# Performance work log

Measured on AMD Instinct MI355X. Metric: run time of the kernel, lower is better.

The kernel has to match this reference:

```python
import jax, jax.numpy as jnp
import numpy as np


def setup_inputs() -> dict:
    key = jax.random.key(0)
    ks = jax.random.split(key, 8)
    B, D_MODEL, H, W, S = 32, 512, 64, 64, 64
    L = H * W
    D_INNER = D_MODEL  # ssd_expand = 1
    x = jax.random.normal(ks[0], (B, D_MODEL, L), jnp.float32)
    # BCdt_proj: Conv1d(d_model -> 3*state_dim, k=1) with bias
    w_bcdt = jax.random.normal(ks[1], (3 * S, D_MODEL), jnp.float32) / np.float32(np.sqrt(D_MODEL))
    b_bcdt = jnp.zeros((3 * S,), jnp.float32)
    # dw_conv: depthwise Conv2d(3*S -> 3*S, k=3, pad=1, groups=3*S) with bias
    w_dw = jax.random.normal(ks[2], (3 * S, 1, 3, 3), jnp.float32) / np.float32(3.0)
    b_dw = jnp.zeros((3 * S,), jnp.float32)
    # hz_proj: Conv1d(d_model -> 2*d_inner, k=1) with bias
    w_hz = jax.random.normal(ks[3], (2 * D_INNER, D_MODEL), jnp.float32) / np.float32(np.sqrt(D_MODEL))
    b_hz = jnp.zeros((2 * D_INNER,), jnp.float32)
    # out_proj: Conv1d(d_inner -> d_model, k=1) with bias
    w_out = jax.random.normal(ks[4], (D_MODEL, D_INNER), jnp.float32) / np.float32(np.sqrt(D_INNER))
    b_out = jnp.zeros((D_MODEL,), jnp.float32)
    A = jax.random.uniform(ks[5], (S,), jnp.float32, minval=1.0, maxval=16.0)
    Dskip = jnp.ones((1,), jnp.float32)
    return {"x": x, "w_bcdt": w_bcdt, "b_bcdt": b_bcdt, "w_dw": w_dw, "b_dw": b_dw,
            "w_hz": w_hz, "b_hz": b_hz, "w_out": w_out, "b_out": b_out,
            "A": A, "Dskip": Dskip, "H": H, "W": W}


def reference(x, w_bcdt, b_bcdt, w_dw, b_dw, w_hz, b_hz, w_out, b_out, A, Dskip, H, W):
    Bn, Cin, L = x.shape
    S = A.shape[0]
    d_inner = w_out.shape[1]
    # pointwise BCdt projection: [B, 3S, L]
    bcdt = jnp.einsum('bcl,oc->bol', x, w_bcdt) + b_bcdt[None, :, None]
    # depthwise 3x3 conv over spatial view
    bcdt = bcdt.reshape(Bn, 3 * S, H, W)
    bcdt = jax.lax.conv_general_dilated(
        bcdt, w_dw, window_strides=(1, 1), padding=((1, 1), (1, 1)),
        dimension_numbers=('NCHW', 'OIHW', 'NCHW'), feature_group_count=3 * S)
    bcdt = bcdt + b_dw[None, :, None, None]
    bcdt = bcdt.reshape(Bn, 3 * S, L)
    Bm, Cm, dt = jnp.split(bcdt, 3, axis=1)  # each [B, S, L]
    Asm = jax.nn.softmax(dt + A[None, :, None], axis=-1)  # softmax over length
    AB = Asm * Bm  # [B, S, L]
    # h = x @ AB^T : [B, d_model, S]
    h = jnp.einsum('bcl,bsl->bcs', x, AB)
    hz = jnp.einsum('bcs,oc->bos', h, w_hz) + b_hz[None, :, None]  # [B, 2*d_inner, S]
    h1, z = jnp.split(hz, 2, axis=1)
    hg = h1 * jax.nn.silu(z) + h1 * Dskip  # gated + D-skip
    ho = jnp.einsum('bcs,oc->bos', hg, w_out) + b_out[None, :, None]  # [B, d_model, S]
    # y = h @ C : [B, d_model, L] -> [B, d_model, H, W]
    y = jnp.einsum('bcs,bsl->bcl', ho, Cm).reshape(Bn, -1, H, W)
    return y, ho
```

## Files before the change

### kernel.cpp

```cpp
#include <hip/hip_runtime.h>

constexpr int BN = 32;
constexpr int DM = 512;
constexpr int SD = 64;
constexpr int LL = 4096;
constexpr int C3 = 192;

#define OUTER16(acc, a4, b4)                                               \
    acc[0][0] += a4.x * b4.x; acc[0][1] += a4.x * b4.y;                    \
    acc[0][2] += a4.x * b4.z; acc[0][3] += a4.x * b4.w;                    \
    acc[1][0] += a4.y * b4.x; acc[1][1] += a4.y * b4.y;                    \
    acc[1][2] += a4.y * b4.z; acc[1][3] += a4.y * b4.w;                    \
    acc[2][0] += a4.z * b4.x; acc[2][1] += a4.z * b4.y;                    \
    acc[2][2] += a4.z * b4.z; acc[2][3] += a4.z * b4.w;                    \
    acc[3][0] += a4.w * b4.x; acc[3][1] += a4.w * b4.y;                    \
    acc[3][2] += a4.w * b4.z; acc[3][3] += a4.w * b4.w;

__global__ __launch_bounds__(256) void k1_bcdt(const float* __restrict__ x,
                                               const float* __restrict__ w,
                                               const float* __restrict__ bias,
                                               float* __restrict__ out) {
    int b = blockIdx.z, o0 = blockIdx.y * 64, l0 = blockIdx.x * 64;
    __shared__ float wl[16][64];
    __shared__ float xl[16][64];
    int t = threadIdx.x;
    int tx = t & 15, ty = t >> 4;
    float acc[4][4] = {};
    const float* xb = x + (size_t)b * DM * LL;
    int oi = t >> 2, kkw = (t & 3) * 4;
    int ci = t >> 4, li = (t & 15) * 4;
    for (int k0 = 0; k0 < DM; k0 += 16) {
        float4 wv = *(const float4*)&w[(size_t)(o0 + oi) * DM + k0 + kkw];
        float4 xv = *(const float4*)&xb[(size_t)(k0 + ci) * LL + l0 + li];
        wl[kkw + 0][oi] = wv.x; wl[kkw + 1][oi] = wv.y;
        wl[kkw + 2][oi] = wv.z; wl[kkw + 3][oi] = wv.w;
        *(float4*)&xl[ci][li] = xv;
        __syncthreads();
#pragma unroll
        for (int kk = 0; kk < 16; ++kk) {
            float4 a4 = *(const float4*)&wl[kk][ty * 4];
            float4 b4 = *(const float4*)&xl[kk][tx * 4];
            OUTER16(acc, a4, b4)
        }
        __syncthreads();
    }
#pragma unroll
    for (int r = 0; r < 4; ++r) {
        float bo = bias[o0 + ty * 4 + r];
        float4 v = make_float4(acc[r][0] + bo, acc[r][1] + bo, acc[r][2] + bo, acc[r][3] + bo);
        *(float4*)&out[((size_t)b * C3 + o0 + ty * 4 + r) * LL + l0 + tx * 4] = v;
    }
}

__global__ __launch_bounds__(256) void k2_conv(float* __restrict__ buf,
                                               const float* __restrict__ wdw,
                                               const float* __restrict__ bdw,
                                               float* __restrict__ cmws) {
    int bc = blockIdx.x;
    int b = bc / C3, ch = bc % C3;
    __shared__ float p[66 * 66];
    int t = threadIdx.x;
    for (int i = t; i < 66 * 66; i += 256) p[i] = 0.f;
    __syncthreads();
    float* plane = buf + (size_t)bc * LL;
    for (int i = t; i < 4096; i += 256) {
        int yy = i >> 6, xx = i & 63;
        p[(yy + 1) * 66 + (xx + 1)] = plane[i];
    }
    __syncthreads();
    float wv[9];
#pragma unroll
    for (int k = 0; k < 9; ++k) wv[k] = wdw[ch * 9 + k];
    float bias = bdw[ch];
    bool is_cm = (ch >= 64 && ch < 128);
    float* cmp = is_cm ? (cmws + ((size_t)b * SD + (ch - 64)) * LL) : nullptr;
    for (int i = t; i < 4096; i += 256) {
        int yy = i >> 6, xx = i & 63;
        float a = bias;
#pragma unroll
        for (int ky = 0; ky < 3; ++ky)
#pragma unroll
            for (int kx = 0; kx < 3; ++kx)
                a += wv[ky * 3 + kx] * p[(yy + ky) * 66 + (xx + kx)];
        plane[i] = a;
        if (is_cm) cmp[i] = a;
    }
}

__global__ __launch_bounds__(256) void k3_softmax(float* __restrict__ conv,
                                                  const float* __restrict__ Ap) {
    int bs = blockIdx.x;
    int b = bs >> 6, s = bs & 63;
    const float* dt = conv + ((size_t)b * C3 + 128 + s) * LL;
    float* bm = conv + ((size_t)b * C3 + s) * LL;
    float Av = Ap[s];
    int t = threadIdx.x;
    float v[16];
    float mx = -1e30f;
#pragma unroll
    for (int j = 0; j < 16; ++j) { v[j] = dt[j * 256 + t] + Av; mx = fmaxf(mx, v[j]); }
#pragma unroll
    for (int off = 32; off >= 1; off >>= 1) mx = fmaxf(mx, __shfl_xor(mx, off, 64));
    __shared__ float redm[4], reds[4];
    int wid = t >> 6, lane = t & 63;
    if (lane == 0) redm[wid] = mx;
    __syncthreads();
    mx = fmaxf(fmaxf(redm[0], redm[1]), fmaxf(redm[2], redm[3]));
    float sum = 0.f;
#pragma unroll
    for (int j = 0; j < 16; ++j) { v[j] = expf(v[j] - mx); sum += v[j]; }
#pragma unroll
    for (int off = 32; off >= 1; off >>= 1) sum += __shfl_xor(sum, off, 64);
    if (lane == 0) reds[wid] = sum;
    __syncthreads();
    sum = reds[0] + reds[1] + reds[2] + reds[3];
    float inv = 1.f / sum;
#pragma unroll
    for (int j = 0; j < 16; ++j) {
        float bmv = bm[j * 256 + t];
        bm[j * 256 + t] = v[j] * inv * bmv;
    }
}

__global__ __launch_bounds__(256) void k4_h(const float* __restrict__ x,
                                            const float* __restrict__ conv,
                                            float* __restrict__ h) {
    int b = blockIdx.y, c0 = blockIdx.x * 64;
    __shared__ float xl[16][64];
    __shared__ float al[16][64];
    int t = threadIdx.x, tx = t & 15, ty = t >> 4;
    float acc[4][4] = {};
    const float* xb = x + (size_t)b * DM * LL;
    const float* abb = conv + (size_t)b * C3 * LL;
    int ri = t >> 2, kk4 = (t & 3) * 4;
    for (int k0 = 0; k0 < LL; k0 += 16) {
        float4 xv = *(const float4*)&xb[(size_t)(c0 + ri) * LL + k0 + kk4];
        float4 av = *(const float4*)&abb[(size_t)ri * LL + k0 + kk4];
        xl[kk4 + 0][ri] = xv.x; xl[kk4 + 1][ri] = xv.y;
        xl[kk4 + 2][ri] = xv.z; xl[kk4 + 3][ri] = xv.w;
        al[kk4 + 0][ri] = av.x; al[kk4 + 1][ri] = av.y;
        al[kk4 + 2][ri] = av.z; al[kk4 + 3][ri] = av.w;
        __syncthreads();
#pragma unroll
        for (int kk = 0; kk < 16; ++kk) {
            float4 a4 = *(const float4*)&xl[kk][ty * 4];
            float4 b4 = *(const float4*)&al[kk][tx * 4];
            OUTER16(acc, a4, b4)
        }
        __syncthreads();
    }
#pragma unroll
    for (int r = 0; r < 4; ++r)
        *(float4*)&h[((size_t)b * DM + c0 + ty * 4 + r) * SD + tx * 4] =
            make_float4(acc[r][0], acc[r][1], acc[r][2], acc[r][3]);
}

__global__ __launch_bounds__(256) void k5_hz_gate(const float* __restrict__ w,
                                                  const float* __restrict__ bias,
                                                  const float* __restrict__ h,
                                                  const float* __restrict__ dskip,
                                                  float* __restrict__ hg) {
    int b = blockIdx.y, o0 = blockIdx.x * 64;
    __shared__ float wl1[16][64];
    __shared__ float wl2[16][64];
    __shared__ float hl[16][64];
    int t = threadIdx.x, tx = t & 15, ty = t >> 4;
    float acc1[4][4] = {}, acc2[4][4] = {};
    const float* hb = h + (size_t)b * DM * SD;
    int oi = t >> 2, kkw = (t & 3) * 4;
    int kh = t >> 4, sh = (t & 15) * 4;
    for (int k0 = 0; k0 < DM; k0 += 16) {
        float4 w1 = *(const float4*)&w[(size_t)(o0 + oi) * DM + k0 + kkw];
        float4 w2 = *(const float4*)&w[(size_t)(o0 + 512 + oi) * DM + k0 + kkw];
        wl1[kkw + 0][oi] = w1.x; wl1[kkw + 1][oi] = w1.y;
        wl1[kkw + 2][oi] = w1.z; wl1[kkw + 3][oi] = w1.w;
        wl2[kkw + 0][oi] = w2.x; wl2[kkw + 1][oi] = w2.y;
        wl2[kkw + 2][oi] = w2.z; wl2[kkw + 3][oi] = w2.w;
        *(float4*)&hl[kh][sh] = *(const float4*)&hb[(size_t)(k0 + kh) * SD + sh];
        __syncthreads();
#pragma unroll
        for (int kk = 0; kk < 16; ++kk) {
            float4 b4 = *(const float4*)&hl[kk][tx * 4];
            float4 a4 = *(const float4*)&wl1[kk][ty * 4];
            OUTER16(acc1, a4, b4)
            float4 c4 = *(const float4*)&wl2[kk][ty * 4];
            OUTER16(acc2, c4, b4)
        }
        __syncthreads();
    }
    float d = dskip[0];
#pragma unroll
    for (int r = 0; r < 4; ++r) {
        int o = o0 + ty * 4 + r;
        float b1 = bias[o], b2 = bias[o + 512];
        float4 v;
        float* vp = &v.x;
#pragma unroll
        for (int j = 0; j < 4; ++j) {
            float h1 = acc1[r][j] + b1;
            float z  = acc2[r][j] + b2;
            float sig = 1.f / (1.f + expf(-z));
            vp[j] = h1 * (z * sig + d);
        }
        *(float4*)&hg[((size_t)b * DM + o) * SD + tx * 4] = v;
    }
}

__global__ __launch_bounds__(256) void k5c_out(const float* __restrict__ w,
                                               const float* __restrict__ bias,
                                               const float* __restrict__ hg,
                                               float* __restrict__ ho_out) {
    int b = blockIdx.y, o0 = blockIdx.x * 64;
    __shared__ float wl[16][64];
    __shared__ float hl[16][64];
    int t = threadIdx.x, tx = t & 15, ty = t >> 4;
    float acc[4][4] = {};
    const float* hb = hg + (size_t)b * DM * SD;
    int oi = t >> 2, kkw = (t & 3) * 4;
    int kh = t >> 4, sh = (t & 15) * 4;
    for (int k0 = 0; k0 < DM; k0 += 16) {
        float4 wv = *(const float4*)&w[(size_t)(o0 + oi) * DM + k0 + kkw];
        wl[kkw + 0][oi] = wv.x; wl[kkw + 1][oi] = wv.y;
        wl[kkw + 2][oi] = wv.z; wl[kkw + 3][oi] = wv.w;
        *(float4*)&hl[kh][sh] = *(const float4*)&hb[(size_t)(k0 + kh) * SD + sh];
        __syncthreads();
#pragma unroll
        for (int kk = 0; kk < 16; ++kk) {
            float4 a4 = *(const float4*)&wl[kk][ty * 4];
            float4 b4 = *(const float4*)&hl[kk][tx * 4];
            OUTER16(acc, a4, b4)
        }
        __syncthreads();
    }
#pragma unroll
    for (int r = 0; r < 4; ++r) {
        int o = o0 + ty * 4 + r;
        float bo = bias[o];
        float4 v = make_float4(acc[r][0] + bo, acc[r][1] + bo, acc[r][2] + bo, acc[r][3] + bo);
        *(float4*)&ho_out[((size_t)b * DM + o) * SD + tx * 4] = v;
    }
}

__global__ __launch_bounds__(256) void k6_y(const float* __restrict__ ho,
                                            const float* __restrict__ cmws,
                                            float* __restrict__ y) {
    int b = blockIdx.z, c0 = blockIdx.y * 64, l0 = blockIdx.x * 64;
    __shared__ float hl[16][64];
    __shared__ float cl[16][64];
    int t = threadIdx.x, tx = t & 15, ty = t >> 4;
    float acc[4][4] = {};
    const float* hb = ho + (size_t)b * DM * SD;
    const float* cm = cmws + (size_t)b * SD * LL;
    int ci = t >> 2, kkh = (t & 3) * 4;
    int kc = t >> 4, li = (t & 15) * 4;
    for (int k0 = 0; k0 < SD; k0 += 16) {
        float4 hv = *(const float4*)&hb[(size_t)(c0 + ci) * SD + k0 + kkh];
        hl[kkh + 0][ci] = hv.x; hl[kkh + 1][ci] = hv.y;
        hl[kkh + 2][ci] = hv.z; hl[kkh + 3][ci] = hv.w;
        *(float4*)&cl[kc][li] = *(const float4*)&cm[(size_t)(k0 + kc) * LL + l0 + li];
        __syncthreads();
#pragma unroll
        for (int kk = 0; kk < 16; ++kk) {
            float4 a4 = *(const float4*)&hl[kk][ty * 4];
            float4 b4 = *(const float4*)&cl[kk][tx * 4];
            OUTER16(acc, a4, b4)
        }
        __syncthreads();
    }
#pragma unroll
    for (int r = 0; r < 4; ++r)
        *(float4*)&y[((size_t)b * DM + c0 + ty * 4 + r) * LL + l0 + tx * 4] =
            make_float4(acc[r][0], acc[r][1], acc[r][2], acc[r][3]);
}

extern "C" void kernel_launch(void* const* d_in, const int* in_sizes, int n_in,
                              void* d_out, int out_size, void* d_ws, size_t ws_size,
                              hipStream_t stream) {
    const float* x      = (const float*)d_in[0];
    const float* w_bcdt = (const float*)d_in[1];
    const float* b_bcdt = (const float*)d_in[2];
    const float* w_dw   = (const float*)d_in[3];
    const float* b_dw   = (const float*)d_in[4];
    const float* w_hz   = (const float*)d_in[5];
    const float* b_hz   = (const float*)d_in[6];
    const float* w_out  = (const float*)d_in[7];
    const float* b_out  = (const float*)d_in[8];
    const float* A      = (const float*)d_in[9];
    const float* Dskip  = (const float*)d_in[10];

    float* y_out  = (float*)d_out;
    float* ho_out = y_out + (size_t)BN * DM * LL;

    float* conv = y_out;

    char* ws = (char*)d_ws;
    float* cmws = (float*)(ws + 0);
    float* h    = (float*)(ws + 33554432);
    float* hg   = (float*)(ws + 37748736);

    k1_bcdt<<<dim3(64, 3, 32), 256, 0, stream>>>(x, w_bcdt, b_bcdt, conv);
    k2_conv<<<dim3(BN * C3), 256, 0, stream>>>(conv, w_dw, b_dw, cmws);
    k3_softmax<<<dim3(BN * SD), 256, 0, stream>>>(conv, A);
    k4_h<<<dim3(8, BN), 256, 0, stream>>>(x, conv, h);
    k5_hz_gate<<<dim3(8, BN), 256, 0, stream>>>(w_hz, b_hz, h, Dskip, hg);
    k5c_out<<<dim3(8, BN), 256, 0, stream>>>(w_out, b_out, hg, ho_out);
    k6_y<<<dim3(64, 8, BN), 256, 0, stream>>>(ho_out, cmws, y_out);
}
```

Measured before the change: 1.149 ms.

## Split-K the h GEMM, enlarge k1 tiles with prefetch, vectorize depthwise conv

The x·AB^T reduction over L is split into 8 partial blocks per (batch, channel tile), with a separate kernel summing the partials. The aim is to fix the original 256-block launch, which underfills the GPU. k1 and k4 now compute 64x128 tiles with register prefetch of the next K slice to hide global latency. The depthwise conv loads and stores float4 and reuses a 3x6 register window per 4 outputs, and it zeroes only the halo. The partial buffer is placed in y_out scratch space that k6 later overwrites, and the split-K adds an extra reduction pass over 8 partial copies.

Result: faster. 1.058 ms (-8.0%).

```diff
diff --git a/kernel.cpp b/kernel.cpp
--- a/kernel.cpp
+++ b/kernel.cpp
@@ -20,35 +20,59 @@
                                                const float* __restrict__ w,
                                                const float* __restrict__ bias,
                                                float* __restrict__ out) {
-    int b = blockIdx.z, o0 = blockIdx.y * 64, l0 = blockIdx.x * 64;
-    __shared__ float wl[16][64];
-    __shared__ float xl[16][64];
+    int b = blockIdx.z, o0 = blockIdx.y * 64, l0 = blockIdx.x * 128;
+    __shared__ float wl[32][68];
+    __shared__ float xl[32][128];
     int t = threadIdx.x;
     int tx = t & 15, ty = t >> 4;
-    float acc[4][4] = {};
+    float acc0[4][4] = {}, acc1[4][4] = {};
     const float* xb = x + (size_t)b * DM * LL;
     int oi = t >> 2, kkw = (t & 3) * 4;
-    int ci = t >> 4, li = (t & 15) * 4;
-    for (int k0 = 0; k0 < DM; k0 += 16) {
-        float4 wv = *(const float4*)&w[(size_t)(o0 + oi) * DM + k0 + kkw];
-        float4 xv = *(const float4*)&xb[(size_t)(k0 + ci) * LL + l0 + li];
-        wl[kkw + 0][oi] = wv.x; wl[kkw + 1][oi] = wv.y;
-        wl[kkw + 2][oi] = wv.z; wl[kkw + 3][oi] = wv.w;
-        *(float4*)&xl[ci][li] = xv;
-        __syncthreads();
-#pragma unroll
-        for (int kk = 0; kk < 16; ++kk) {
+    int ci = t >> 5, li = (t & 31) * 4;
+    float4 wv0 = *(const float4*)&w[(size_t)(o0 + oi) * DM + kkw];
+    float4 wv1 = *(const float4*)&w[(size_t)(o0 + oi) * DM + kkw + 16];
+    float4 xv0 = *(const float4*)&xb[(size_t)(ci +  0) * LL + l0 + li];
+    float4 xv1 = *(const float4*)&xb[(size_t)(ci +  8) * LL + l0 + li];
+    float4 xv2 = *(const float4*)&xb[(size_t)(ci + 16) * LL + l0 + li];
+    float4 xv3 = *(const float4*)&xb[(size_t)(ci + 24) * LL + l0 + li];
+    for (int k0 = 0; k0 < DM; k0 += 32) {
+        wl[kkw +  0][oi] = wv0.x; wl[kkw +  1][oi] = wv0.y;
+        wl[kkw +  2][oi] = wv0.z; wl[kkw +  3][oi] = wv0.w;
+        wl[kkw + 16][oi] = wv1.x; wl[kkw + 17][oi] = wv1.y;
+        wl[kkw + 18][oi] = wv1.z; wl[kkw + 19][oi] = wv1.w;
+        *(float4*)&xl[ci +  0][li] = xv0;
+        *(float4*)&xl[ci +  8][li] = xv1;
+        *(float4*)&xl[ci + 16][li] = xv2;
+        *(float4*)&xl[ci + 24][li] = xv3;
+        __syncthreads();
+        if (k0 + 32 < DM) {
+            const float* wp = &w[(size_t)(o0 + oi) * DM + k0 + 32 + kkw];
+            wv0 = *(const float4*)wp;
+            wv1 = *(const float4*)(wp + 16);
+            const float* xp = &xb[(size_t)(k0 + 32 + ci) * LL + l0 + li];
+            xv0 = *(const float4*)xp;
+            xv1 = *(const float4*)(xp + (size_t)8 * LL);
+            xv2 = *(const float4*)(xp + (size_t)16 * LL);
+            xv3 = *(const float4*)(xp + (size_t)24 * LL);
+        }
+#pragma unroll
+        for (int kk = 0; kk < 32; ++kk) {
             float4 a4 = *(const float4*)&wl[kk][ty * 4];
             float4 b4 = *(const float4*)&xl[kk][tx * 4];
-            OUTER16(acc, a4, b4)
+            float4 c4 = *(const float4*)&xl[kk][64 + tx * 4];
+            OUTER16(acc0, a4, b4)
+            OUTER16(acc1, a4, c4)
         }
         __syncthreads();
     }
 #pragma unroll
     for (int r = 0; r < 4; ++r) {
         float bo = bias[o0 + ty * 4 + r];
-        float4 v = make_float4(acc[r][0] + bo, acc[r][1] + bo, acc[r][2] + bo, acc[r][3] + bo);
-        *(float4*)&out[((size_t)b * C3 + o0 + ty * 4 + r) * LL + l0 + tx * 4] = v;
+        float* op = &out[((size_t)b * C3 + o0 + ty * 4 + r) * LL + l0];
+        *(float4*)&op[tx * 4] =
+            make_float4(acc0[r][0] + bo, acc0[r][1] + bo, acc0[r][2] + bo, acc0[r][3] + bo);
+        *(float4*)&op[64 + tx * 4] =
+            make_float4(acc1[r][0] + bo, acc1[r][1] + bo, acc1[r][2] + bo, acc1[r][3] + bo);
     }
 }
 
@@ -60,12 +84,15 @@
     int b = bc / C3, ch = bc % C3;
     __shared__ float p[66 * 66];
     int t = threadIdx.x;
-    for (int i = t; i < 66 * 66; i += 256) p[i] = 0.f;
-    __syncthreads();
+    for (int i = t; i < 66; i += 256) { p[i] = 0.f; p[65 * 66 + i] = 0.f; }
+    for (int i = t; i < 64; i += 256) { p[(i + 1) * 66] = 0.f; p[(i + 1) * 66 + 65] = 0.f; }
     float* plane = buf + (size_t)bc * LL;
-    for (int i = t; i < 4096; i += 256) {
-        int yy = i >> 6, xx = i & 63;
-        p[(yy + 1) * 66 + (xx + 1)] = plane[i];
+    const float4* plane4 = (const float4*)plane;
+    for (int i = t; i < 1024; i += 256) {
+        float4 v = plane4[i];
+        int yy = i >> 4, xx = (i & 15) << 2;
+        float* dst = &p[(yy + 1) * 66 + xx + 1];
+        dst[0] = v.x; dst[1] = v.y; dst[2] = v.z; dst[3] = v.w;
     }
     __syncthreads();
     float wv[9];
@@ -74,16 +101,26 @@
     float bias = bdw[ch];
     bool is_cm = (ch >= 64 && ch < 128);
     float* cmp = is_cm ? (cmws + ((size_t)b * SD + (ch - 64)) * LL) : nullptr;
-    for (int i = t; i < 4096; i += 256) {
-        int yy = i >> 6, xx = i & 63;
-        float a = bias;
-#pragma unroll
-        for (int ky = 0; ky < 3; ++ky)
-#pragma unroll
-            for (int kx = 0; kx < 3; ++kx)
-                a += wv[ky * 3 + kx] * p[(yy + ky) * 66 + (xx + kx)];
-        plane[i] = a;
-        if (is_cm) cmp[i] = a;
+    for (int i = t; i < 1024; i += 256) {
+        int yy = i >> 4, xx = (i & 15) << 2;
+        float r0[6], r1[6], r2[6];
+#pragma unroll
+        for (int j = 0; j < 6; ++j) {
+            r0[j] = p[(yy + 0) * 66 + xx + j];
+            r1[j] = p[(yy + 1) * 66 + xx + j];
+            r2[j] = p[(yy + 2) * 66 + xx + j];
+        }
+        float4 o;
+        float* op = &o.x;
+#pragma unroll
+        for (int j = 0; j < 4; ++j) {
+            op[j] = bias
+                  + wv[0] * r0[j] + wv[1] * r0[j + 1] + wv[2] * r0[j + 2]
+                  + wv[3] * r1[j] + wv[4] * r1[j + 1] + wv[5] * r1[j + 2]
+                  + wv[6] * r2[j] + wv[7] * r2[j + 1] + wv[8] * r2[j + 2];
+        }
+        ((float4*)plane)[i] = o;
+        if (is_cm) ((float4*)cmp)[i] = o;
     }
 }
 
@@ -122,37 +159,68 @@
     }
 }
 
+constexpr int KP = 512;
+constexpr size_t HP_STRIDE = (size_t)BN * DM * SD;
 __global__ __launch_bounds__(256) void k4_h(const float* __restrict__ x,
                                             const float* __restrict__ conv,
-                                            float* __restrict__ h) {
-    int b = blockIdx.y, c0 = blockIdx.x * 64;
-    __shared__ float xl[16][64];
-    __shared__ float al[16][64];
+                                            float* __restrict__ hpart) {
+    int b = blockIdx.z, c0 = blockIdx.x * 128, part = blockIdx.y;
+    int kbeg = part * KP;
+    __shared__ float xl[16][132];
+    __shared__ float al[16][68];
     int t = threadIdx.x, tx = t & 15, ty = t >> 4;
-    float acc[4][4] = {};
+    float acc0[4][4] = {}, acc1[4][4] = {};
     const float* xb = x + (size_t)b * DM * LL;
     const float* abb = conv + (size_t)b * C3 * LL;
     int ri = t >> 2, kk4 = (t & 3) * 4;
-    for (int k0 = 0; k0 < LL; k0 += 16) {
-        float4 xv = *(const float4*)&xb[(size_t)(c0 + ri) * LL + k0 + kk4];
-        float4 av = *(const float4*)&abb[(size_t)ri * LL + k0 + kk4];
-        xl[kk4 + 0][ri] = xv.x; xl[kk4 + 1][ri] = xv.y;
-        xl[kk4 + 2][ri] = xv.z; xl[kk4 + 3][ri] = xv.w;
+    float4 xv0 = *(const float4*)&xb[(size_t)(c0 + ri) * LL + kbeg + kk4];
+    float4 xv1 = *(const float4*)&xb[(size_t)(c0 + 64 + ri) * LL + kbeg + kk4];
+    float4 av  = *(const float4*)&abb[(size_t)ri * LL + kbeg + kk4];
+    for (int k0 = kbeg; k0 < kbeg + KP; k0 += 16) {
+        xl[kk4 + 0][ri] = xv0.x; xl[kk4 + 1][ri] = xv0.y;
+        xl[kk4 + 2][ri] = xv0.z; xl[kk4 + 3][ri] = xv0.w;
+        xl[kk4 + 0][64 + ri] = xv1.x; xl[kk4 + 1][64 + ri] = xv1.y;
+        xl[kk4 + 2][64 + ri] = xv1.z; xl[kk4 + 3][64 + ri] = xv1.w;
         al[kk4 + 0][ri] = av.x; al[kk4 + 1][ri] = av.y;
         al[kk4 + 2][ri] = av.z; al[kk4 + 3][ri] = av.w;
         __syncthreads();
+        if (k0 + 16 < kbeg + KP) {
+            xv0 = *(const float4*)&xb[(size_t)(c0 + ri) * LL + k0 + 16 + kk4];
+            xv1 = *(const float4*)&xb[(size_t)(c0 + 64 + ri) * LL + k0 + 16 + kk4];
+            av  = *(const float4*)&abb[(size_t)ri * LL + k0 + 16 + kk4];
+        }
 #pragma unroll
         for (int kk = 0; kk < 16; ++kk) {
             float4 a4 = *(const float4*)&xl[kk][ty * 4];
+            float4 c4 = *(const float4*)&xl[kk][64 + ty * 4];
             float4 b4 = *(const float4*)&al[kk][tx * 4];
-            OUTER16(acc, a4, b4)
-        }
-        __syncthreads();
-    }
-#pragma unroll
-    for (int r = 0; r < 4; ++r)
-        *(float4*)&h[((size_t)b * DM + c0 + ty * 4 + r) * SD + tx * 4] =
-            make_float4(acc[r][0], acc[r][1], acc[r][2], acc[r][3]);
+            OUTER16(acc0, a4, b4)
+            OUTER16(acc1, c4, b4)
+        }
+        __syncthreads();
+    }
+    float* hp = hpart + (size_t)part * HP_STRIDE;
+#pragma unroll
+    for (int r = 0; r < 4; ++r) {
+        *(float4*)&hp[((size_t)b * DM + c0 + ty * 4 + r) * SD + tx * 4] =
+            make_float4(acc0[r][0], acc0[r][1], acc0[r][2], acc0[r][3]);
+        *(float4*)&hp[((size_t)b * DM + c0 + 64 + ty * 4 + r) * SD + tx * 4] =
+            make_float4(acc1[r][0], acc1[r][1], acc1[r][2], acc1[r][3]);
+    }
+}
+
+__global__ __launch_bounds__(256) void k4r(const float* __restrict__ hpart,
+                                           float* __restrict__ h) {
+    size_t i = (size_t)blockIdx.x * 256 + threadIdx.x;
+    const float4* hp = (const float4*)hpart;
+    constexpr size_t PS = HP_STRIDE / 4;
+    float4 a = hp[i];
+#pragma unroll
+    for (int p = 1; p < 8; ++p) {
+        float4 v = hp[i + (size_t)p * PS];
+        a.x += v.x; a.y += v.y; a.z += v.z; a.w += v.w;
+    }
+    ((float4*)h)[i] = a;
 }
 
 __global__ __launch_bounds__(256) void k5_hz_gate(const float* __restrict__ w,
@@ -293,15 +361,18 @@
 
     float* conv = y_out;
 
+    float* hpart = y_out + (size_t)33554432;
+
     char* ws = (char*)d_ws;
     float* cmws = (float*)(ws + 0);
     float* h    = (float*)(ws + 33554432);
     float* hg   = (float*)(ws + 37748736);
 
-    k1_bcdt<<<dim3(64, 3, 32), 256, 0, stream>>>(x, w_bcdt, b_bcdt, conv);
+    k1_bcdt<<<dim3(32, 3, 32), 256, 0, stream>>>(x, w_bcdt, b_bcdt, conv);
     k2_conv<<<dim3(BN * C3), 256, 0, stream>>>(conv, w_dw, b_dw, cmws);
     k3_softmax<<<dim3(BN * SD), 256, 0, stream>>>(conv, A);
-    k4_h<<<dim3(8, BN), 256, 0, stream>>>(x, conv, h);
+    k4_h<<<dim3(4, 8, BN), 256, 0, stream>>>(x, conv, hpart);
+    k4r<<<dim3(1024), 256, 0, stream>>>(hpart, h);
     k5_hz_gate<<<dim3(8, BN), 256, 0, stream>>>(w_hz, b_hz, h, Dskip, hg);
     k5c_out<<<dim3(8, BN), 256, 0, stream>>>(w_out, b_out, hg, ho_out);
     k6_y<<<dim3(64, 8, BN), 256, 0, stream>>>(ho_out, cmws, y_out);
```

## Rewrite pipeline with 8x8 register tiles, split-K h GEMM, fused conv+softmax

Applied to the files above, without the earlier changes.

Nearly every kernel is rewritten. The GEMMs (bcdt projection, h, y) now use 8x8 per-thread register tiles with swizzled, padded shared memory and register prefetch of the next K slice. The h reduction is split along L into 16 partial sums plus a separate reduce kernel, so many more blocks run at once. The depthwise conv and softmax are fused into one kernel per (b,s), removing a round trip of the plane through global memory. The gate is moved into the out-projection's load. Partial sums and hz scratch live inside the y output buffer, which is only overwritten later, and the extra reduce pass adds memory traffic.

Result: slower. 1.220 ms (+6.2%).

```diff
diff --git a/kernel.cpp b/kernel.cpp
--- a/kernel.cpp
+++ b/kernel.cpp
@@ -16,206 +16,281 @@
     acc[3][0] += a4.w * b4.x; acc[3][1] += a4.w * b4.y;                    \
     acc[3][2] += a4.w * b4.z; acc[3][3] += a4.w * b4.w;
 
+#define OUTER64(acc, a0, a1, b0, b1)                                       \
+    {                                                                      \
+        float af[8] = {a0.x, a0.y, a0.z, a0.w, a1.x, a1.y, a1.z, a1.w};    \
+        float bf[8] = {b0.x, b0.y, b0.z, b0.w, b1.x, b1.y, b1.z, b1.w};    \
+        _Pragma("unroll")                                                  \
+        for (int i_ = 0; i_ < 8; ++i_)                                     \
+            _Pragma("unroll")                                              \
+            for (int j_ = 0; j_ < 8; ++j_) acc[i_][j_] += af[i_] * bf[j_]; \
+    }
+
 __global__ __launch_bounds__(256) void k1_bcdt(const float* __restrict__ x,
                                                const float* __restrict__ w,
                                                const float* __restrict__ bias,
                                                float* __restrict__ out) {
-    int b = blockIdx.z, o0 = blockIdx.y * 64, l0 = blockIdx.x * 64;
-    __shared__ float wl[16][64];
-    __shared__ float xl[16][64];
+    int o0 = blockIdx.x * 64;
+    int l0 = blockIdx.y * 256;
+    int b  = blockIdx.z;
+    __shared__ float  wl[16][68];
+    __shared__ float4 xl4[16][66];
     int t = threadIdx.x;
-    int tx = t & 15, ty = t >> 4;
-    float acc[4][4] = {};
+    int tx = t & 31, ty = t >> 5;
+    float acc[8][8] = {};
     const float* xb = x + (size_t)b * DM * LL;
-    int oi = t >> 2, kkw = (t & 3) * 4;
-    int ci = t >> 4, li = (t & 15) * 4;
+
+    int wo = t & 63, wk = t >> 6;
+    int kr = t >> 4, cbase = t & 15;
+    int wpos[4];
+#pragma unroll
+    for (int j = 0; j < 4; ++j) {
+        int cb = cbase + 16 * j, pb = cb >> 1;
+        wpos[j] = ((pb ^ ((pb >> 2) & 3)) << 1) | (cb & 1);
+    }
+    int rp = (tx ^ ((tx >> 2) & 3)) * 2;
+
+    float4 wv = *(const float4*)&w[(size_t)(o0 + wo) * DM + wk * 4];
+    float4 xv[4];
+#pragma unroll
+    for (int j = 0; j < 4; ++j)
+        xv[j] = *(const float4*)&xb[(size_t)kr * LL + l0 + (cbase + 16 * j) * 4];
+
     for (int k0 = 0; k0 < DM; k0 += 16) {
-        float4 wv = *(const float4*)&w[(size_t)(o0 + oi) * DM + k0 + kkw];
-        float4 xv = *(const float4*)&xb[(size_t)(k0 + ci) * LL + l0 + li];
-        wl[kkw + 0][oi] = wv.x; wl[kkw + 1][oi] = wv.y;
-        wl[kkw + 2][oi] = wv.z; wl[kkw + 3][oi] = wv.w;
-        *(float4*)&xl[ci][li] = xv;
-        __syncthreads();
+        wl[wk * 4 + 0][wo] = wv.x; wl[wk * 4 + 1][wo] = wv.y;
+        wl[wk * 4 + 2][wo] = wv.z; wl[wk * 4 + 3][wo] = wv.w;
+#pragma unroll
+        for (int j = 0; j < 4; ++j) xl4[kr][wpos[j]] = xv[j];
+        __syncthreads();
+        if (k0 + 16 < DM) {
+            wv = *(const float4*)&w[(size_t)(o0 + wo) * DM + k0 + 16 + wk * 4];
+#pragma unroll
+            for (int j = 0; j < 4; ++j)
+                xv[j] = *(const float4*)&xb[(size_t)(k0 + 16 + kr) * LL + l0 + (cbase + 16 * j) * 4];
+        }
 #pragma unroll
         for (int kk = 0; kk < 16; ++kk) {
-            float4 a4 = *(const float4*)&wl[kk][ty * 4];
-            float4 b4 = *(const float4*)&xl[kk][tx * 4];
-            OUTER16(acc, a4, b4)
-        }
-        __syncthreads();
-    }
-#pragma unroll
-    for (int r = 0; r < 4; ++r) {
-        float bo = bias[o0 + ty * 4 + r];
-        float4 v = make_float4(acc[r][0] + bo, acc[r][1] + bo, acc[r][2] + bo, acc[r][3] + bo);
-        *(float4*)&out[((size_t)b * C3 + o0 + ty * 4 + r) * LL + l0 + tx * 4] = v;
-    }
-}
-
-__global__ __launch_bounds__(256) void k2_conv(float* __restrict__ buf,
-                                               const float* __restrict__ wdw,
-                                               const float* __restrict__ bdw,
-                                               float* __restrict__ cmws) {
-    int bc = blockIdx.x;
-    int b = bc / C3, ch = bc % C3;
+            float4 a0 = *(const float4*)&wl[kk][ty * 8];
+            float4 a1 = *(const float4*)&wl[kk][ty * 8 + 4];
+            float4 b0 = xl4[kk][rp];
+            float4 b1 = xl4[kk][rp + 1];
+            OUTER64(acc, a0, a1, b0, b1)
+        }
+        __syncthreads();
+    }
+#pragma unroll
+    for (int i = 0; i < 8; ++i) {
+        int o = o0 + ty * 8 + i;
+        float bo = bias[o];
+        float* op = &out[((size_t)b * C3 + o) * LL + l0 + tx * 8];
+        *(float4*)&op[0] = make_float4(acc[i][0] + bo, acc[i][1] + bo, acc[i][2] + bo, acc[i][3] + bo);
+        *(float4*)&op[4] = make_float4(acc[i][4] + bo, acc[i][5] + bo, acc[i][6] + bo, acc[i][7] + bo);
+    }
+}
+
+__device__ __forceinline__ void load_plane(const float* __restrict__ plane, float* p, int t) {
+    const float4* p4 = (const float4*)plane;
+    for (int i = t; i < 1024; i += 256) {
+        float4 v = p4[i];
+        int yy = i >> 4, xx = (i & 15) << 2;
+        float* dst = &p[(yy + 1) * 66 + xx + 1];
+        dst[0] = v.x; dst[1] = v.y; dst[2] = v.z; dst[3] = v.w;
+    }
+}
+
+__device__ __forceinline__ void conv_plane(const float* p, const float* wv, float bias,
+                                           int t, float4* out4) {
+#pragma unroll
+    for (int g = 0; g < 4; ++g) {
+        int fi = g * 256 + t;
+        int yy = fi >> 4, xx = (fi & 15) << 2;
+        float r0[6], r1[6], r2[6];
+#pragma unroll
+        for (int j = 0; j < 6; ++j) {
+            r0[j] = p[(yy + 0) * 66 + xx + j];
+            r1[j] = p[(yy + 1) * 66 + xx + j];
+            r2[j] = p[(yy + 2) * 66 + xx + j];
+        }
+        float* op = (float*)&out4[g];
+#pragma unroll
+        for (int j = 0; j < 4; ++j)
+            op[j] = bias + wv[0] * r0[j] + wv[1] * r0[j + 1] + wv[2] * r0[j + 2]
+                         + wv[3] * r1[j] + wv[4] * r1[j + 1] + wv[5] * r1[j + 2]
+                         + wv[6] * r2[j] + wv[7] * r2[j + 1] + wv[8] * r2[j + 2];
+    }
+}
+
+__global__ __launch_bounds__(256) void k2_fused(float* __restrict__ buf,
+                                                const float* __restrict__ wdw,
+                                                const float* __restrict__ bdw,
+                                                const float* __restrict__ Ap,
+                                                float* __restrict__ cmws) {
+    int s = blockIdx.x, b = blockIdx.y;
     __shared__ float p[66 * 66];
+    __shared__ float redm[4], reds[4];
     int t = threadIdx.x;
-    for (int i = t; i < 66 * 66; i += 256) p[i] = 0.f;
-    __syncthreads();
-    float* plane = buf + (size_t)bc * LL;
-    for (int i = t; i < 4096; i += 256) {
-        int yy = i >> 6, xx = i & 63;
-        p[(yy + 1) * 66 + (xx + 1)] = plane[i];
-    }
-    __syncthreads();
-    float wv[9];
-#pragma unroll
-    for (int k = 0; k < 9; ++k) wv[k] = wdw[ch * 9 + k];
-    float bias = bdw[ch];
-    bool is_cm = (ch >= 64 && ch < 128);
-    float* cmp = is_cm ? (cmws + ((size_t)b * SD + (ch - 64)) * LL) : nullptr;
-    for (int i = t; i < 4096; i += 256) {
-        int yy = i >> 6, xx = i & 63;
-        float a = bias;
-#pragma unroll
-        for (int ky = 0; ky < 3; ++ky)
-#pragma unroll
-            for (int kx = 0; kx < 3; ++kx)
-                a += wv[ky * 3 + kx] * p[(yy + ky) * 66 + (xx + kx)];
-        plane[i] = a;
-        if (is_cm) cmp[i] = a;
-    }
-}
-
-__global__ __launch_bounds__(256) void k3_softmax(float* __restrict__ conv,
-                                                  const float* __restrict__ Ap) {
-    int bs = blockIdx.x;
-    int b = bs >> 6, s = bs & 63;
-    const float* dt = conv + ((size_t)b * C3 + 128 + s) * LL;
-    float* bm = conv + ((size_t)b * C3 + s) * LL;
+    for (int i = t; i < 66; i += 256) { p[i] = 0.f; p[65 * 66 + i] = 0.f; }
+    for (int i = t; i < 64; i += 256) { p[(i + 1) * 66] = 0.f; p[(i + 1) * 66 + 65] = 0.f; }
+
+    const float* base = buf + (size_t)b * C3 * LL;
+    float wvB[9], wvC[9], wvD[9];
+#pragma unroll
+    for (int k = 0; k < 9; ++k) {
+        wvB[k] = wdw[(size_t)s * 9 + k];
+        wvC[k] = wdw[(size_t)(64 + s) * 9 + k];
+        wvD[k] = wdw[(size_t)(128 + s) * 9 + k];
+    }
+    float4 bm4[4], cm4[4], dt4[4];
+
+    load_plane(base + (size_t)s * LL, p, t);
+    __syncthreads();
+    conv_plane(p, wvB, bdw[s], t, bm4);
+    __syncthreads();
+    load_plane(base + (size_t)(64 + s) * LL, p, t);
+    __syncthreads();
+    conv_plane(p, wvC, bdw[64 + s], t, cm4);
+    __syncthreads();
+    {
+        float4* cmp4 = (float4*)(cmws + ((size_t)b * SD + s) * LL);
+#pragma unroll
+        for (int g = 0; g < 4; ++g) cmp4[g * 256 + t] = cm4[g];
+    }
+    load_plane(base + (size_t)(128 + s) * LL, p, t);
+    __syncthreads();
+    conv_plane(p, wvD, bdw[128 + s], t, dt4);
+
     float Av = Ap[s];
-    int t = threadIdx.x;
-    float v[16];
     float mx = -1e30f;
 #pragma unroll
-    for (int j = 0; j < 16; ++j) { v[j] = dt[j * 256 + t] + Av; mx = fmaxf(mx, v[j]); }
+    for (int g = 0; g < 4; ++g) {
+        float* v = (float*)&dt4[g];
+#pragma unroll
+        for (int j = 0; j < 4; ++j) { v[j] += Av; mx = fmaxf(mx, v[j]); }
+    }
 #pragma unroll
     for (int off = 32; off >= 1; off >>= 1) mx = fmaxf(mx, __shfl_xor(mx, off, 64));
-    __shared__ float redm[4], reds[4];
     int wid = t >> 6, lane = t & 63;
     if (lane == 0) redm[wid] = mx;
     __syncthreads();
     mx = fmaxf(fmaxf(redm[0], redm[1]), fmaxf(redm[2], redm[3]));
     float sum = 0.f;
 #pragma unroll
-    for (int j = 0; j < 16; ++j) { v[j] = expf(v[j] - mx); sum += v[j]; }
+    for (int g = 0; g < 4; ++g) {
+        float* v = (float*)&dt4[g];
+#pragma unroll
+        for (int j = 0; j < 4; ++j) { v[j] = expf(v[j] - mx); sum += v[j]; }
+    }
 #pragma unroll
     for (int off = 32; off >= 1; off >>= 1) sum += __shfl_xor(sum, off, 64);
     if (lane == 0) reds[wid] = sum;
     __syncthreads();
     sum = reds[0] + reds[1] + reds[2] + reds[3];
     float inv = 1.f / sum;
-#pragma unroll
-    for (int j = 0; j < 16; ++j) {
-        float bmv = bm[j * 256 + t];
-        bm[j * 256 + t] = v[j] * inv * bmv;
-    }
-}
-
+    float4* abp4 = (float4*)(buf + ((size_t)b * C3 + s) * LL);
+#pragma unroll
+    for (int g = 0; g < 4; ++g) {
+        float4 bm = bm4[g], dt = dt4[g], o;
+        o.x = dt.x * inv * bm.x; o.y = dt.y * inv * bm.y;
+        o.z = dt.z * inv * bm.z; o.w = dt.w * inv * bm.w;
+        abp4[g * 256 + t] = o;
+    }
+}
+
+constexpr int KP4 = 256;
+constexpr size_t HP_STRIDE = (size_t)BN * DM * SD;
 __global__ __launch_bounds__(256) void k4_h(const float* __restrict__ x,
                                             const float* __restrict__ conv,
-                                            float* __restrict__ h) {
-    int b = blockIdx.y, c0 = blockIdx.x * 64;
-    __shared__ float xl[16][64];
-    __shared__ float al[16][64];
-    int t = threadIdx.x, tx = t & 15, ty = t >> 4;
-    float acc[4][4] = {};
+                                            float* __restrict__ hpart) {
+    int c0 = blockIdx.x * 256;
+    int part = blockIdx.y;
+    int b = blockIdx.z;
+    int kbeg = part * KP4;
+    __shared__ float xlf[16][264];
+    __shared__ float al[16][68];
+    int t = threadIdx.x;
+    int tc = t & 31, ts = t >> 5;
+    float acc[8][8] = {};
     const float* xb = x + (size_t)b * DM * LL;
     const float* abb = conv + (size_t)b * C3 * LL;
-    int ri = t >> 2, kk4 = (t & 3) * 4;
-    for (int k0 = 0; k0 < LL; k0 += 16) {
-        float4 xv = *(const float4*)&xb[(size_t)(c0 + ri) * LL + k0 + kk4];
-        float4 av = *(const float4*)&abb[(size_t)ri * LL + k0 + kk4];
-        xl[kk4 + 0][ri] = xv.x; xl[kk4 + 1][ri] = xv.y;
-        xl[kk4 + 2][ri] = xv.z; xl[kk4 + 3][ri] = xv.w;
-        al[kk4 + 0][ri] = av.x; al[kk4 + 1][ri] = av.y;
-        al[kk4 + 2][ri] = av.z; al[kk4 + 3][ri] = av.w;
-        __syncthreads();
+
+    int cr = t >> 2, lj = t & 3;
+    int ep[4];
+#pragma unroll
+    for (int j = 0; j < 4; ++j) {
+        int c = cr + 64 * j;
+        int cb = c >> 2, pb = cb >> 1;
+        ep[j] = ((((pb ^ ((pb >> 2) & 3)) << 1) | (cb & 1)) << 2) + (c & 3);
+    }
+    int rp = (tc ^ ((tc >> 2) & 3)) * 2;
+
+    float4 xv[4];
+#pragma unroll
+    for (int j = 0; j < 4; ++j)
+        xv[j] = *(const float4*)&xb[(size_t)(c0 + cr + 64 * j) * LL + kbeg + lj * 4];
+    float4 av = *(const float4*)&abb[(size_t)cr * LL + kbeg + lj * 4];
+
+    for (int k0 = kbeg; k0 < kbeg + KP4; k0 += 16) {
+#pragma unroll
+        for (int j = 0; j < 4; ++j) {
+            xlf[lj * 4 + 0][ep[j]] = xv[j].x;
+            xlf[lj * 4 + 1][ep[j]] = xv[j].y;
+            xlf[lj * 4 + 2][ep[j]] = xv[j].z;
+            xlf[lj * 4 + 3][ep[j]] = xv[j].w;
+        }
+        al[lj * 4 + 0][cr] = av.x;
+        al[lj * 4 + 1][cr] = av.y;
+        al[lj * 4 + 2][cr] = av.z;
+        al[lj * 4 + 3][cr] = av.w;
+        __syncthreads();
+        if (k0 + 16 < kbeg + KP4) {
+#pragma unroll
+            for (int j = 0; j < 4; ++j)
+                xv[j] = *(const float4*)&xb[(size_t)(c0 + cr + 64 * j) * LL + k0 + 16 + lj * 4];
+            av = *(const float4*)&abb[(size_t)cr * LL + k0 + 16 + lj * 4];
+        }
 #pragma unroll
         for (int kk = 0; kk < 16; ++kk) {
-            float4 a4 = *(const float4*)&xl[kk][ty * 4];
-            float4 b4 = *(const float4*)&al[kk][tx * 4];
-            OUTER16(acc, a4, b4)
-        }
-        __syncthreads();
-    }
-#pragma unroll
-    for (int r = 0; r < 4; ++r)
-        *(float4*)&h[((size_t)b * DM + c0 + ty * 4 + r) * SD + tx * 4] =
-            make_float4(acc[r][0], acc[r][1], acc[r][2], acc[r][3]);
-}
-
-__global__ __launch_bounds__(256) void k5_hz_gate(const float* __restrict__ w,
-                                                  const float* __restrict__ bias,
-                                                  const float* __restrict__ h,
-                                                  const float* __restrict__ dskip,
-                                                  float* __restrict__ hg) {
-    int b = blockIdx.y, o0 = blockIdx.x * 64;
-    __shared__ float wl1[16][64];
-    __shared__ float wl2[16][64];
-    __shared__ float hl[16][64];
-    int t = threadIdx.x, tx = t & 15, ty = t >> 4;
-    float acc1[4][4] = {}, acc2[4][4] = {};
-    const float* hb = h + (size_t)b * DM * SD;
-    int oi = t >> 2, kkw = (t & 3) * 4;
-    int kh = t >> 4, sh = (t & 15) * 4;
-    for (int k0 = 0; k0 < DM; k0 += 16) {
-        float4 w1 = *(const float4*)&w[(size_t)(o0 + oi) * DM + k0 + kkw];
-        float4 w2 = *(const float4*)&w[(size_t)(o0 + 512 + oi) * DM + k0 + kkw];
-        wl1[kkw + 0][oi] = w1.x; wl1[kkw + 1][oi] = w1.y;
-        wl1[kkw + 2][oi] = w1.z; wl1[kkw + 3][oi] = w1.w;
-        wl2[kkw + 0][oi] = w2.x; wl2[kkw + 1][oi] = w2.y;
-        wl2[kkw + 2][oi] = w2.z; wl2[kkw + 3][oi] = w2.w;
-        *(float4*)&hl[kh][sh] = *(const float4*)&hb[(size_t)(k0 + kh) * SD + sh];
-        __syncthreads();
-#pragma unroll
-        for (int kk = 0; kk < 16; ++kk) {
-            float4 b4 = *(const float4*)&hl[kk][tx * 4];
-            float4 a4 = *(const float4*)&wl1[kk][ty * 4];
-            OUTER16(acc1, a4, b4)
-            float4 c4 = *(const float4*)&wl2[kk][ty * 4];
-            OUTER16(acc2, c4, b4)
-        }
-        __syncthreads();
-    }
-    float d = dskip[0];
-#pragma unroll
-    for (int r = 0; r < 4; ++r) {
-        int o = o0 + ty * 4 + r;
-        float b1 = bias[o], b2 = bias[o + 512];
-        float4 v;
-        float* vp = &v.x;
-#pragma unroll
-        for (int j = 0; j < 4; ++j) {
-            float h1 = acc1[r][j] + b1;
-            float z  = acc2[r][j] + b2;
-            float sig = 1.f / (1.f + expf(-z));
-            vp[j] = h1 * (z * sig + d);
-        }
-        *(float4*)&hg[((size_t)b * DM + o) * SD + tx * 4] = v;
-    }
-}
-
-__global__ __launch_bounds__(256) void k5c_out(const float* __restrict__ w,
-                                               const float* __restrict__ bias,
-                                               const float* __restrict__ hg,
-                                               float* __restrict__ ho_out) {
+            float4 a0 = *(const float4*)&xlf[kk][rp * 4];
+            float4 a1 = *(const float4*)&xlf[kk][rp * 4 + 4];
+            float4 b0 = *(const float4*)&al[kk][ts * 8];
+            float4 b1 = *(const float4*)&al[kk][ts * 8 + 4];
+            OUTER64(acc, a0, a1, b0, b1)
+        }
+        __syncthreads();
+    }
+    float* hp = hpart + (size_t)part * HP_STRIDE + (size_t)b * DM * SD;
+#pragma unroll
+    for (int i = 0; i < 8; ++i) {
+        float* row = &hp[(size_t)(c0 + tc * 8 + i) * SD + ts * 8];
+        *(float4*)&row[0] = make_float4(acc[i][0], acc[i][1], acc[i][2], acc[i][3]);
+        *(float4*)&row[4] = make_float4(acc[i][4], acc[i][5], acc[i][6], acc[i][7]);
+    }
+}
+
+__global__ __launch_bounds__(256) void k4r(const float* __restrict__ hpart,
+                                           float* __restrict__ h) {
+    size_t i = (size_t)blockIdx.x * 256 + threadIdx.x;
+    const float4* hp = (const float4*)hpart;
+    constexpr size_t PS = HP_STRIDE / 4;
+    float4 a = hp[i];
+#pragma unroll
+    for (int p = 1; p < 16; ++p) {
+        float4 v = hp[i + (size_t)p * PS];
+        a.x += v.x; a.y += v.y; a.z += v.z; a.w += v.w;
+    }
+    ((float4*)h)[i] = a;
+}
+
+__global__ __launch_bounds__(256) void k5_hz(const float* __restrict__ w,
+                                             const float* __restrict__ bias,
+                                             const float* __restrict__ h,
+                                             float* __restrict__ hz) {
     int b = blockIdx.y, o0 = blockIdx.x * 64;
     __shared__ float wl[16][64];
     __shared__ float hl[16][64];
     int t = threadIdx.x, tx = t & 15, ty = t >> 4;
     float acc[4][4] = {};
-    const float* hb = hg + (size_t)b * DM * SD;
+    const float* hb = h + (size_t)b * DM * SD;
     int oi = t >> 2, kkw = (t & 3) * 4;
     int kh = t >> 4, sh = (t & 15) * 4;
     for (int k0 = 0; k0 < DM; k0 += 16) {
@@ -236,41 +311,108 @@
     for (int r = 0; r < 4; ++r) {
         int o = o0 + ty * 4 + r;
         float bo = bias[o];
-        float4 v = make_float4(acc[r][0] + bo, acc[r][1] + bo, acc[r][2] + bo, acc[r][3] + bo);
-        *(float4*)&ho_out[((size_t)b * DM + o) * SD + tx * 4] = v;
+        *(float4*)&hz[((size_t)b * 1024 + o) * SD + tx * 4] =
+            make_float4(acc[r][0] + bo, acc[r][1] + bo, acc[r][2] + bo, acc[r][3] + bo);
+    }
+}
+
+__global__ __launch_bounds__(256) void k5c_gate(const float* __restrict__ w,
+                                                const float* __restrict__ bias,
+                                                const float* __restrict__ hz,
+                                                const float* __restrict__ dskip,
+                                                float* __restrict__ ho_out) {
+    int b = blockIdx.y, o0 = blockIdx.x * 64;
+    __shared__ float wl[16][64];
+    __shared__ float hl[16][64];
+    int t = threadIdx.x, tx = t & 15, ty = t >> 4;
+    float acc[4][4] = {};
+    const float* hzb = hz + (size_t)b * 1024 * SD;
+    float d = dskip[0];
+    int oi = t >> 2, kkw = (t & 3) * 4;
+    int kh = t >> 4, sh = (t & 15) * 4;
+    for (int k0 = 0; k0 < DM; k0 += 16) {
+        float4 wv = *(const float4*)&w[(size_t)(o0 + oi) * DM + k0 + kkw];
+        wl[kkw + 0][oi] = wv.x; wl[kkw + 1][oi] = wv.y;
+        wl[kkw + 2][oi] = wv.z; wl[kkw + 3][oi] = wv.w;
+        float4 h1 = *(const float4*)&hzb[(size_t)(k0 + kh) * SD + sh];
+        float4 zz = *(const float4*)&hzb[(size_t)(512 + k0 + kh) * SD + sh];
+        float4 g;
+        g.x = h1.x * (zz.x / (1.f + expf(-zz.x)) + d);
+        g.y = h1.y * (zz.y / (1.f + expf(-zz.y)) + d);
+        g.z = h1.z * (zz.z / (1.f + expf(-zz.z)) + d);
+        g.w = h1.w * (zz.w / (1.f + expf(-zz.w)) + d);
+        *(float4*)&hl[kh][sh] = g;
+        __syncthreads();
+#pragma unroll
+        for (int kk = 0; kk < 16; ++kk) {
+            float4 a4 = *(const float4*)&wl[kk][ty * 4];
+            float4 b4 = *(const float4*)&hl[kk][tx * 4];
+            OUTER16(acc, a4, b4)
+        }
+        __syncthreads();
+    }
+#pragma unroll
+    for (int r = 0; r < 4; ++r) {
+        int o = o0 + ty * 4 + r;
+        float bo = bias[o];
+        *(float4*)&ho_out[((size_t)b * DM + o) * SD + tx * 4] =
+            make_float4(acc[r][0] + bo, acc[r][1] + bo, acc[r][2] + bo, acc[r][3] + bo);
     }
 }
 
 __global__ __launch_bounds__(256) void k6_y(const float* __restrict__ ho,
                                             const float* __restrict__ cmws,
                                             float* __restrict__ y) {
-    int b = blockIdx.z, c0 = blockIdx.y * 64, l0 = blockIdx.x * 64;
-    __shared__ float hl[16][64];
-    __shared__ float cl[16][64];
-    int t = threadIdx.x, tx = t & 15, ty = t >> 4;
-    float acc[4][4] = {};
+    int c0 = blockIdx.x * 128;
+    int l0 = blockIdx.y * 128;
+    int b = blockIdx.z;
+    __shared__ float hl[16][132];
+    __shared__ float clf[16][136];
+    int t = threadIdx.x;
+    int tcol = t & 15, trow = t >> 4;
+    float acc[8][8] = {};
     const float* hb = ho + (size_t)b * DM * SD;
     const float* cm = cmws + (size_t)b * SD * LL;
-    int ci = t >> 2, kkh = (t & 3) * 4;
-    int kc = t >> 4, li = (t & 15) * 4;
+    int cr = t & 127, kj = t >> 7;
+    int krr = t >> 4, ch = t & 15;
+    int wp0 = (ch ^ ((ch >> 2) & 3)) * 2;
+    int rp = (tcol ^ ((tcol >> 2) & 3)) * 2;
+
+    float4 hv0 = *(const float4*)&hb[(size_t)(c0 + cr) * SD + kj * 8];
+    float4 hv1 = *(const float4*)&hb[(size_t)(c0 + cr) * SD + kj * 8 + 4];
+    float4 cv0 = *(const float4*)&cm[(size_t)krr * LL + l0 + ch * 8];
+    float4 cv1 = *(const float4*)&cm[(size_t)krr * LL + l0 + ch * 8 + 4];
+
     for (int k0 = 0; k0 < SD; k0 += 16) {
-        float4 hv = *(const float4*)&hb[(size_t)(c0 + ci) * SD + k0 + kkh];
-        hl[kkh + 0][ci] = hv.x; hl[kkh + 1][ci] = hv.y;
-        hl[kkh + 2][ci] = hv.z; hl[kkh + 3][ci] = hv.w;
-        *(float4*)&cl[kc][li] = *(const float4*)&cm[(size_t)(k0 + kc) * LL + l0 + li];
-        __syncthreads();
+        hl[kj * 8 + 0][cr] = hv0.x; hl[kj * 8 + 1][cr] = hv0.y;
+        hl[kj * 8 + 2][cr] = hv0.z; hl[kj * 8 + 3][cr] = hv0.w;
+        hl[kj * 8 + 4][cr] = hv1.x; hl[kj * 8 + 5][cr] = hv1.y;
+        hl[kj * 8 + 6][cr] = hv1.z; hl[kj * 8 + 7][cr] = hv1.w;
+        *(float4*)&clf[krr][wp0 * 4] = cv0;
+        *(float4*)&clf[krr][wp0 * 4 + 4] = cv1;
+        __syncthreads();
+        if (k0 + 16 < SD) {
+            hv0 = *(const float4*)&hb[(size_t)(c0 + cr) * SD + k0 + 16 + kj * 8];
+            hv1 = *(const float4*)&hb[(size_t)(c0 + cr) * SD + k0 + 16 + kj * 8 + 4];
+            cv0 = *(const float4*)&cm[(size_t)(k0 + 16 + krr) * LL + l0 + ch * 8];
+            cv1 = *(const float4*)&cm[(size_t)(k0 + 16 + krr) * LL + l0 + ch * 8 + 4];
+        }
 #pragma unroll
         for (int kk = 0; kk < 16; ++kk) {
-            float4 a4 = *(const float4*)&hl[kk][ty * 4];
-            float4 b4 = *(const float4*)&cl[kk][tx * 4];
-            OUTER16(acc, a4, b4)
-        }
-        __syncthreads();
-    }
-#pragma unroll
-    for (int r = 0; r < 4; ++r)
-        *(float4*)&y[((size_t)b * DM + c0 + ty * 4 + r) * LL + l0 + tx * 4] =
-            make_float4(acc[r][0], acc[r][1], acc[r][2], acc[r][3]);
+            float4 a0 = *(const float4*)&hl[kk][trow * 8];
+            float4 a1 = *(const float4*)&hl[kk][trow * 8 + 4];
+            float4 b0 = *(const float4*)&clf[kk][rp * 4];
+            float4 b1 = *(const float4*)&clf[kk][rp * 4 + 4];
+            OUTER64(acc, a0, a1, b0, b1)
+        }
+        __syncthreads();
+    }
+#pragma unroll
+    for (int i = 0; i < 8; ++i) {
+        float* row = &y[((size_t)b * DM + c0 + trow * 8 + i) * LL + l0 + tcol * 8];
+        *(float4*)&row[0] = make_float4(acc[i][0], acc[i][1], acc[i][2], acc[i][3]);
+        *(float4*)&row[4] = make_float4(acc[i][4], acc[i][5], acc[i][6], acc[i][7]);
+    }
 }
 
 extern "C" void kernel_launch(void* const* d_in, const int* in_sizes, int n_in,
@@ -291,18 +433,19 @@
     float* y_out  = (float*)d_out;
     float* ho_out = y_out + (size_t)BN * DM * LL;
 
-    float* conv = y_out;
+    float* conv  = y_out;
+    float* hpart = y_out + (size_t)33554432;
+    float* hz    = y_out + (size_t)52428800;
 
     char* ws = (char*)d_ws;
     float* cmws = (float*)(ws + 0);
     float* h    = (float*)(ws + 33554432);
-    float* hg   = (float*)(ws + 37748736);
-
-    k1_bcdt<<<dim3(64, 3, 32), 256, 0, stream>>>(x, w_bcdt, b_bcdt, conv);
-    k2_conv<<<dim3(BN * C3), 256, 0, stream>>>(conv, w_dw, b_dw, cmws);
-    k3_softmax<<<dim3(BN * SD), 256, 0, stream>>>(conv, A);
-    k4_h<<<dim3(8, BN), 256, 0, stream>>>(x, conv, h);
-    k5_hz_gate<<<dim3(8, BN), 256, 0, stream>>>(w_hz, b_hz, h, Dskip, hg);
-    k5c_out<<<dim3(8, BN), 256, 0, stream>>>(w_out, b_out, hg, ho_out);
-    k6_y<<<dim3(64, 8, BN), 256, 0, stream>>>(ho_out, cmws, y_out);
-}
+
+    k1_bcdt <<<dim3(3, 16, BN), 256, 0, stream>>>(x, w_bcdt, b_bcdt, conv);
+    k2_fused<<<dim3(SD, BN),    256, 0, stream>>>(conv, w_dw, b_dw, A, cmws);
+    k4_h    <<<dim3(2, 16, BN), 256, 0, stream>>>(x, conv, hpart);
+    k4r     <<<dim3(1024),      256, 0, stream>>>(hpart, h);
+    k5_hz   <<<dim3(16, BN),    256, 0, stream>>>(w_hz, b_hz, h, hz);
+    k5c_gate<<<dim3(8, BN),     256, 0, stream>>>(w_out, b_out, hz, Dskip, ho_out);
+    k6_y    <<<dim3(4, 32, BN), 256, 0, stream>>>(ho_out, cmws, y_out);
+}
```
